# Kernel tuning notes

Hardware: AMD Instinct MI355X
Metric: run time of the kernel (lower is better)

The kernel has to match this reference:

```python
import jax, jax.numpy as jnp
import numpy as np

N, E, F_IN, HID, EMB = 100000, 3200000, 128, 16, 8
NEG_SLOPE = 0.2


def _seg_softmax(logits, seg, n):
    # Numerically stable softmax over segments (per trailing channel if 2D).
    m = jax.ops.segment_max(logits, seg, num_segments=n)
    e = jnp.exp(logits - m[seg])
    s = jax.ops.segment_sum(e, seg, num_segments=n)
    return e / s[seg]


def _gatv2(x, src, dst, Wl, Wr, att, bias, t, n):
    # GATv2Conv, heads=1, add_self_loops=False, eval mode (dropout off),
    # with learnable SoftmaxAggregation replacing the sum aggregation.
    xl = x @ Wl                      # [N, C] source transform
    xr = x @ Wr                      # [N, C] target transform
    score = jnp.sum(jax.nn.leaky_relu(xl[src] + xr[dst], NEG_SLOPE) * att, axis=-1)  # [E]
    alpha = _seg_softmax(score, dst, n)          # attention softmax over incoming edges
    m = xl[src] * alpha[:, None]                 # [E, C] messages
    w = _seg_softmax(m * t, dst, n)              # SoftmaxAggregation(learn=True), per channel
    return jax.ops.segment_sum(w * m, dst, num_segments=n) + bias


def setup_inputs() -> dict:
    key = jax.random.key(0)
    ks = iter(jax.random.split(key, 32))
    r = lambda shape, s=0.1: jax.random.normal(next(ks), shape, dtype=jnp.float32) * s
    return dict(
        x=r((N, F_IN), 1.0),
        edge_index=jax.random.randint(next(ks), (2, E), 0, N, dtype=jnp.int32),
        batch=jnp.arange(N, dtype=jnp.int32),
        Wl1=r((F_IN, HID)), Wr1=r((F_IN, HID)), att1=r((HID,)), b1=r((HID,)),
        Wlin1=r((F_IN, HID)), blin1=r((HID,)),
        Wl2=r((HID, EMB)), Wr2=r((HID, EMB)), att2=r((EMB,)), b2=r((EMB,)),
        Wlin2=r((HID, EMB)), blin2=r((EMB,)),
        t=jnp.ones((1,), jnp.float32),
        W3=r((EMB, EMB)), b3=r((EMB,)),
        W4=r((EMB, 1)), b4=r((1,)),
        W5=r((1, 1)), b5=r((1,)),
        Wout=r((1, 1)), bout=r((1,)),
    )


def reference(x, edge_index, batch, Wl1, Wr1, att1, b1, Wlin1, blin1,
              Wl2, Wr2, att2, b2, Wlin2, blin2, t,
              W3, b3, W4, b4, W5, b5, Wout, bout):
    n = x.shape[0]
    src, dst = edge_index[0], edge_index[1]
    # layer 1: GATv2 + skip Linear, relu, global_add_pool
    h = _gatv2(x, src, dst, Wl1, Wr1, att1, b1, t, n) + (x @ Wlin1 + blin1)
    h = jax.nn.relu(h)
    g = jax.ops.segment_sum(h, batch, num_segments=n)  # global_add_pool (batch=arange(N))
    # layer 2: GATv2 + skip Linear on pooled tensor (as in original code), relu, pool
    h2 = _gatv2(g, src, dst, Wl2, Wr2, att2, b2, t, n) + (g @ Wlin2 + blin2)
    h2 = jax.nn.relu(h2)
    g2 = jax.ops.segment_sum(h2, batch, num_segments=n)
    # small MLP head
    z = jax.nn.relu(g2 @ W3 + b3)
    z = jax.nn.relu(z @ W4 + b4)
    z = jax.nn.relu(z @ W5 + b5)
    return jax.nn.log_sigmoid(z @ Wout + bout)
```

## Files before the change

kernel.cpp:

```cpp
#include <hip/hip_runtime.h>
#include <hip/hip_bf16.h>
#include <math.h>

#define F_IN 128
#define C1 16
#define C2 8

#define LBITS 8
#define LOCAL (1 << LBITS)
#define NB_MAX 512
#define ITEMS 16
#define EPB (256 * ITEMS)
#define HISTBLK 512

static __device__ __forceinline__ unsigned short f2bf(float f) {
  __hip_bfloat16 h = __float2bfloat16(f);
  return *(unsigned short*)&h;
}

__global__ __launch_bounds__(256) void hist_gemm(
    const int* __restrict__ dst, int* __restrict__ bcount, int E, int NB,
    const float* __restrict__ x, const float* __restrict__ Wl, const float* __restrict__ Wr,
    const float* __restrict__ Wlin, const float* __restrict__ blin,
    __hip_bfloat16* __restrict__ XLh, float* __restrict__ XR, float* __restrict__ SK, int N) {
  if (blockIdx.x < HISTBLK) {
    __shared__ int h[NB_MAX];
    for (int i = threadIdx.x; i < NB; i += blockDim.x) h[i] = 0;
    __syncthreads();
    int stride = HISTBLK * 256;
    int tid = blockIdx.x * 256 + threadIdx.x;
    if ((E & 3) == 0) {
      const int4* d4 = (const int4*)dst;
      int n4 = E >> 2;
      for (int i = tid; i < n4; i += stride) {
        int4 d = d4[i];
        atomicAdd(&h[d.x >> LBITS], 1);
        atomicAdd(&h[d.y >> LBITS], 1);
        atomicAdd(&h[d.z >> LBITS], 1);
        atomicAdd(&h[d.w >> LBITS], 1);
      }
    } else {
      for (int e = tid; e < E; e += stride) atomicAdd(&h[dst[e] >> LBITS], 1);
    }
    __syncthreads();
    for (int i = threadIdx.x; i < NB; i += blockDim.x)
      if (h[i]) atomicAdd(&bcount[i], h[i]);
  } else {
    int bx = blockIdx.x - HISTBLK;
    int mat = bx % 3;
    int node = (bx / 3) * 256 + threadIdx.x;
    if (node >= N) return;
    const float* __restrict__ W = (mat == 0) ? Wl : (mat == 1) ? Wr : Wlin;
    const float4* xr4 = (const float4*)(x + (size_t)node * F_IN);
    float acc[16];
#pragma unroll
    for (int c = 0; c < 16; c++) acc[c] = 0.f;
#pragma unroll 8
    for (int kk = 0; kk < F_IN / 4; kk++) {
      float4 xv = xr4[kk];
      float xs[4] = {xv.x, xv.y, xv.z, xv.w};
#pragma unroll
      for (int j = 0; j < 4; j++) {
        int k = kk * 4 + j;
#pragma unroll
        for (int c = 0; c < 16; c++) acc[c] = fmaf(xs[j], W[k * 16 + c], acc[c]);
      }
    }
    if (mat == 0) {
      unsigned int pk[8];
#pragma unroll
      for (int i = 0; i < 8; i++)
        pk[i] = (unsigned)f2bf(acc[2 * i]) | ((unsigned)f2bf(acc[2 * i + 1]) << 16);
      uint4* xlp = (uint4*)(XLh + (size_t)node * 16);
      xlp[0] = make_uint4(pk[0], pk[1], pk[2], pk[3]);
      xlp[1] = make_uint4(pk[4], pk[5], pk[6], pk[7]);
    } else if (mat == 1) {
      float4* xrp = (float4*)(XR + (size_t)node * 16);
#pragma unroll
      for (int q = 0; q < 4; q++)
        xrp[q] = make_float4(acc[4 * q], acc[4 * q + 1], acc[4 * q + 2], acc[4 * q + 3]);
    } else {
      float4* skp = (float4*)(SK + (size_t)node * 16);
#pragma unroll
      for (int q = 0; q < 4; q++)
        skp[q] = make_float4(acc[4 * q] + blin[4 * q], acc[4 * q + 1] + blin[4 * q + 1],
                             acc[4 * q + 2] + blin[4 * q + 2], acc[4 * q + 3] + blin[4 * q + 3]);
    }
  }
}

__global__ void bucket_scan(const int* __restrict__ bcount, int* __restrict__ bbase,
                            int* __restrict__ bcursor, int NB) {
  __shared__ int sd[NB_MAX];
  int t = threadIdx.x;
  int v = (t < NB) ? bcount[t] : 0;
  sd[t] = v;
  __syncthreads();
  int acc = v;
  for (int off = 1; off < NB_MAX; off <<= 1) {
    int u = (t >= off) ? sd[t - off] : 0;
    __syncthreads();
    acc += u;
    sd[t] = acc;
    __syncthreads();
  }
  if (t < NB) {
    int excl = acc - v;
    bbase[t] = excl;
    bcursor[t] = excl;
    if (t == NB - 1) bbase[NB] = acc;
  }
}

__global__ __launch_bounds__(256) void phaseA_lds(const int* __restrict__ src,
                                                  const int* __restrict__ dst,
                                                  int* __restrict__ bcursor,
                                                  int* __restrict__ packed, int E, int NB) {
  __shared__ int hist[NB_MAX];
  __shared__ int lbase[NB_MAX];
  __shared__ int gbase[NB_MAX];
  __shared__ int sdata[256];
  __shared__ int stage[EPB];
  __shared__ unsigned short stageb[EPB];
  int t = threadIdx.x;
  for (int i = t; i < NB; i += 256) hist[i] = 0;
  __syncthreads();
  int base = blockIdx.x * EPB;
  int vals[ITEMS];
  int bkt[ITEMS];
  bool vec = ((E & 3) == 0) && (base + EPB <= E);
  if (vec) {
    const int4* s4 = (const int4*)(src + base);
    const int4* d4 = (const int4*)(dst + base);
#pragma unroll
    for (int q = 0; q < ITEMS / 4; q++) {
      int idx = q * 256 + t;
      int4 sv = s4[idx];
      int4 dv = d4[idx];
      int ss[4] = {sv.x, sv.y, sv.z, sv.w};
      int dd[4] = {dv.x, dv.y, dv.z, dv.w};
#pragma unroll
      for (int r = 0; r < 4; r++) {
        int k = q * 4 + r;
        bkt[k] = dd[r] >> LBITS;
        vals[k] = (ss[r] << LBITS) | (dd[r] & (LOCAL - 1));
        atomicAdd(&hist[bkt[k]], 1);
      }
    }
  } else {
#pragma unroll
    for (int k = 0; k < ITEMS; k++) {
      int e = base + k * 256 + t;
      if (e < E) {
        int s = src[e];
        int d = dst[e];
        bkt[k] = d >> LBITS;
        vals[k] = (s << LBITS) | (d & (LOCAL - 1));
        atomicAdd(&hist[bkt[k]], 1);
      } else {
        bkt[k] = -1;
      }
    }
  }
  __syncthreads();
  int i0 = 2 * t, i1 = 2 * t + 1;
  int h0 = (i0 < NB) ? hist[i0] : 0;
  int h1 = (i1 < NB) ? hist[i1] : 0;
  int s2 = h0 + h1;
  sdata[t] = s2;
  __syncthreads();
  int acc = s2;
  for (int off = 1; off < 256; off <<= 1) {
    int u = (t >= off) ? sdata[t - off] : 0;
    __syncthreads();
    acc += u;
    sdata[t] = acc;
    __syncthreads();
  }
  int excl = acc - s2;
  if (i0 < NB) lbase[i0] = excl;
  if (i1 < NB) lbase[i1] = excl + h0;
  __syncthreads();
  for (int i = t; i < NB; i += 256) {
    int c = hist[i];
    gbase[i] = c ? atomicAdd(&bcursor[i], c) : 0;
    hist[i] = lbase[i];
  }
  __syncthreads();
  if (vec) {
#pragma unroll
    for (int k = 0; k < ITEMS; k++) {
      int lp = atomicAdd(&hist[bkt[k]], 1);
      stage[lp] = vals[k];
      stageb[lp] = (unsigned short)bkt[k];
    }
  } else {
#pragma unroll
    for (int k = 0; k < ITEMS; k++) {
      if (bkt[k] >= 0) {
        int lp = atomicAdd(&hist[bkt[k]], 1);
        stage[lp] = vals[k];
        stageb[lp] = (unsigned short)bkt[k];
      }
    }
  }
  __syncthreads();
  int blockE = E - base;
  if (blockE > EPB) blockE = EPB;
  for (int i = t; i < blockE; i += 256) {
    int b = stageb[i];
    packed[gbase[b] + (i - lbase[b])] = stage[i];
  }
}

__global__ void phaseB_sort(const int* __restrict__ packed, const int* __restrict__ bbase,
                            int* __restrict__ row_ptr, int* __restrict__ ssrc, int N, int E) {
  __shared__ int h[LOCAL];
  __shared__ int sd[LOCAL];
  int b = blockIdx.x;
  int t = threadIdx.x;
  int beg = bbase[b], end = bbase[b + 1];
  int node0 = b << LBITS;
  h[t] = 0;
  __syncthreads();
  for (int j = beg + t; j < end; j += blockDim.x) atomicAdd(&h[packed[j] & (LOCAL - 1)], 1);
  __syncthreads();
  int cnt = h[t];
  sd[t] = cnt;
  __syncthreads();
  int acc = cnt;
  for (int off = 1; off < LOCAL; off <<= 1) {
    int u = (t >= off) ? sd[t - off] : 0;
    __syncthreads();
    acc += u;
    sd[t] = acc;
    __syncthreads();
  }
  int myex = acc - cnt;
  int node = node0 + t;
  if (node < N) row_ptr[node] = beg + myex;
  h[t] = beg + myex;
  if (b == gridDim.x - 1 && t == 0) row_ptr[N] = E;
  __syncthreads();
  for (int j = beg + t; j < end; j += blockDim.x) {
    int v = packed[j];
    int l = v & (LOCAL - 1);
    int p = atomicAdd(&h[l], 1);
    ssrc[p] = ((v >> LBITS) << 5) | (l & 31);
  }
}

template <int C, int POOL, bool HEAD, bool FUSEG2>
__global__ __launch_bounds__(256) void gat_layer(
    const __hip_bfloat16* __restrict__ XLh, const float* __restrict__ XR,
    const float* __restrict__ SK, const float* __restrict__ att, const float* __restrict__ bias,
    const float* __restrict__ tp, const int* __restrict__ row_ptr, const int* __restrict__ ssrc,
    float* __restrict__ H, int N,
    const float* __restrict__ P0, const float* __restrict__ P1, const float* __restrict__ P2,
    const float* __restrict__ P3, const float* __restrict__ P4, const float* __restrict__ P5,
    const float* __restrict__ P6, const float* __restrict__ P7,
    __hip_bfloat16* __restrict__ XL2h, float* __restrict__ XR2, float* __restrict__ SK2,
    float* __restrict__ out) {
  constexpr int NPB = 256 / C;
  __shared__ __align__(16) unsigned short vpool[POOL * C];
  __shared__ float ppool[POOL];
  __shared__ __align__(16) float xrl[NPB * C];
  __shared__ int nb[NPB + 1];
  __shared__ float wfuse[FUSEG2 ? 392 : 1];
  float* hsh = (float*)vpool;
  int t = threadIdx.x;
  int node0 = blockIdx.x * NPB;

  if (t <= NPB) {
    int nd = node0 + t;
    nb[t] = row_ptr[(nd < N) ? nd : N];
  }
  {
    size_t xi = (size_t)node0 * C + t;
    xrl[t] = (xi < (size_t)N * C) ? XR[xi] : 0.f;
  }
  if constexpr (FUSEG2) {
    for (int i = t; i < 392; i += 256)
      wfuse[i] = (i < 128) ? P0[i] : (i < 256) ? P1[i - 128] : (i < 384) ? P2[i - 256] : P3[i - 384];
  }
  float attr[C];
#pragma unroll
  for (int cc = 0; cc < C; cc++) attr[cc] = att[cc];
  float tval = tp[0];
  __syncthreads();

  int bbeg = nb[0];
  int nE = nb[NPB] - bbeg;
  int nCap = (nE < POOL) ? nE : POOL;
  const unsigned short* XLu = (const unsigned short*)XLh;

  for (int slot = t; slot < nCap; slot += 256) {
    int sp = ssrc[bbeg + slot];
    int s = sp >> 5;
    int g = sp & (NPB - 1);
    float v[C];
    if constexpr (C == 16) {
      const uint4* gp = (const uint4*)(XLu + (size_t)s * 16);
      uint4 a = gp[0], b = gp[1];
      *(uint4*)&vpool[slot * 16] = a;
      *(uint4*)&vpool[slot * 16 + 8] = b;
      unsigned arr[8] = {a.x, a.y, a.z, a.w, b.x, b.y, b.z, b.w};
#pragma unroll
      for (int i = 0; i < 8; i++) {
        v[2 * i] = __uint_as_float(arr[i] << 16);
        v[2 * i + 1] = __uint_as_float(arr[i] & 0xffff0000u);
      }
    } else {
      const uint4* gp = (const uint4*)(XLu + (size_t)s * 8);
      uint4 a = gp[0];
      *(uint4*)&vpool[slot * 8] = a;
      unsigned arr[4] = {a.x, a.y, a.z, a.w};
#pragma unroll
      for (int i = 0; i < 4; i++) {
        v[2 * i] = __uint_as_float(arr[i] << 16);
        v[2 * i + 1] = __uint_as_float(arr[i] & 0xffff0000u);
      }
    }
    float xr[C];
    const float4* xp = (const float4*)&xrl[g * C];
#pragma unroll
    for (int q = 0; q < C / 4; q++) {
      float4 f = xp[q];
      xr[4 * q] = f.x;
      xr[4 * q + 1] = f.y;
      xr[4 * q + 2] = f.z;
      xr[4 * q + 3] = f.w;
    }
    float p0 = 0.f, p1 = 0.f, p2 = 0.f, p3 = 0.f;
#pragma unroll
    for (int cc = 0; cc < C; cc += 4) {
      float u0 = v[cc] + xr[cc];
      float u1 = v[cc + 1] + xr[cc + 1];
      float u2 = v[cc + 2] + xr[cc + 2];
      float u3 = v[cc + 3] + xr[cc + 3];
      p0 = fmaf(fmaxf(u0, 0.2f * u0), attr[cc], p0);
      p1 = fmaf(fmaxf(u1, 0.2f * u1), attr[cc + 1], p1);
      p2 = fmaf(fmaxf(u2, 0.2f * u2), attr[cc + 2], p2);
      p3 = fmaf(fmaxf(u3, 0.2f * u3), attr[cc + 3], p3);
    }
    ppool[slot] = __expf((p0 + p1) + (p2 + p3));
  }
  __syncthreads();

  int g = t / C;
  int c = t % C;
  int base = nb[g] - bbeg;
  int deg = nb[g + 1] - nb[g];
  int capd = POOL - base;
  capd = capd < 0 ? 0 : (capd > deg ? deg : capd);

  float invS0;
  {
    float s0 = 0.f;
    for (int j = c; j < capd; j += C) s0 += ppool[base + j];
    for (int j = capd + c; j < deg; j += C) {
      int s = ssrc[bbeg + base + j] >> 5;
      float sc = 0.f;
#pragma unroll
      for (int cc = 0; cc < C; cc++) {
        float v = __bfloat162float(XLh[(size_t)s * C + cc]);
        float u = v + xrl[g * C + cc];
        sc = fmaf(fmaxf(u, 0.2f * u), attr[cc], sc);
      }
      s0 += __expf(sc);
    }
#pragma unroll
    for (int m = 1; m < C; m <<= 1) s0 += __shfl_xor(s0, m, C);
    invS0 = (deg > 0) ? 1.0f / s0 : 0.f;
  }
  float a = invS0 * tval;

  float S1 = 0.f, S2 = 0.f, S1b = 0.f, S2b = 0.f;
  int jj = 0;
  for (; jj + 2 <= capd; jj += 2) {
    int sl0 = base + jj;
    float v0 = __uint_as_float(((unsigned)vpool[sl0 * C + c]) << 16);
    float q0 = v0 * ppool[sl0] * a;
    float v1 = __uint_as_float(((unsigned)vpool[(sl0 + 1) * C + c]) << 16);
    float q1 = v1 * ppool[sl0 + 1] * a;
    float w0 = __expf(q0);
    float w1 = __expf(q1);
    S1 += w0;
    S2 = fmaf(w0, q0, S2);
    S1b += w1;
    S2b = fmaf(w1, q1, S2b);
  }
  for (; jj < capd; jj++) {
    int sl = base + jj;
    float v = __uint_as_float(((unsigned)vpool[sl * C + c]) << 16);
    float q = v * ppool[sl] * a;
    float w = __expf(q);
    S1 += w;
    S2 = fmaf(w, q, S2);
  }
  for (; jj < deg; jj++) {
    int s = ssrc[bbeg + base + jj] >> 5;
    float sc = 0.f, vc = 0.f;
#pragma unroll
    for (int cc = 0; cc < C; cc++) {
      float v = __bfloat162float(XLh[(size_t)s * C + cc]);
      if (cc == c) vc = v;
      float u = v + xrl[g * C + cc];
      sc = fmaf(fmaxf(u, 0.2f * u), attr[cc], sc);
    }
    float p = __expf(sc);
    float q = vc * p * a;
    float w = __expf(q);
    S1 += w;
    S2 = fmaf(w, q, S2);
  }
  S1 += S1b;
  S2 += S2b;

  int node = node0 + g;
  bool valid = node < N;
  float hval = 0.f;
  if (valid) {
    float td = (tval != 0.f) ? tval : 1.f;
    float gat = (deg > 0) ? (S2 / (S1 * td)) : 0.f;
    hval = fmaxf(gat + bias[c] + SK[(size_t)node * C + c], 0.f);
  }
  if constexpr (FUSEG2) {
    __syncthreads();
    hsh[g * C + c] = hval;
    __syncthreads();
    if (t < NPB * 8) {
      int g2 = t >> 3, c2 = t & 7;
      int nd = node0 + g2;
      if (nd < N) {
        float a0 = 0.f, a1 = 0.f, a2 = 0.f;
#pragma unroll
        for (int k = 0; k < 16; k++) {
          float hv = hsh[g2 * 16 + k];
          a0 = fmaf(hv, wfuse[k * 8 + c2], a0);
          a1 = fmaf(hv, wfuse[128 + k * 8 + c2], a1);
          a2 = fmaf(hv, wfuse[256 + k * 8 + c2], a2);
        }
        ((unsigned short*)XL2h)[(size_t)nd * 8 + c2] = f2bf(a0);
        XR2[(size_t)nd * 8 + c2] = a1;
        SK2[(size_t)nd * 8 + c2] = a2 + wfuse[384 + c2];
      }
    }
  } else if constexpr (HEAD) {
    __syncthreads();
    hsh[g * C + c] = hval;
    __syncthreads();
    if (t < NPB) {
      int nd = node0 + t;
      if (nd < N) {
        float h[8];
#pragma unroll
        for (int k = 0; k < 8; k++) h[k] = hsh[t * 8 + k];
        float s4 = 0.f;
#pragma unroll
        for (int cc = 0; cc < 8; cc++) {
          float z = P1[cc];
#pragma unroll
          for (int k = 0; k < 8; k++) z = fmaf(h[k], P0[k * 8 + cc], z);
          z = fmaxf(z, 0.f);
          s4 = fmaf(z, P2[cc], s4);
        }
        s4 = fmaxf(s4 + P3[0], 0.f);
        float s5 = fmaxf(fmaf(s4, P4[0], P5[0]), 0.f);
        float zo = fmaf(s5, P6[0], P7[0]);
        float ls;
        if (zo >= 0.f)
          ls = -log1pf(expf(-zo));
        else
          ls = zo - log1pf(expf(zo));
        out[nd] = ls;
      }
    }
  } else {
    if (valid) H[(size_t)node * C + c] = hval;
  }
}

extern "C" void kernel_launch(void* const* d_in, const int* in_sizes, int n_in,
                              void* d_out, int out_size, void* d_ws, size_t ws_size,
                              hipStream_t stream) {
  const float* x = (const float*)d_in[0];
  const int* ei = (const int*)d_in[1];
  const float* Wl1 = (const float*)d_in[3];
  const float* Wr1 = (const float*)d_in[4];
  const float* att1 = (const float*)d_in[5];
  const float* b1 = (const float*)d_in[6];
  const float* Wlin1 = (const float*)d_in[7];
  const float* blin1 = (const float*)d_in[8];
  const float* Wl2 = (const float*)d_in[9];
  const float* Wr2 = (const float*)d_in[10];
  const float* att2 = (const float*)d_in[11];
  const float* b2 = (const float*)d_in[12];
  const float* Wlin2 = (const float*)d_in[13];
  const float* blin2 = (const float*)d_in[14];
  const float* t = (const float*)d_in[15];
  const float* W3 = (const float*)d_in[16];
  const float* b3 = (const float*)d_in[17];
  const float* W4 = (const float*)d_in[18];
  const float* b4 = (const float*)d_in[19];
  const float* W5 = (const float*)d_in[20];
  const float* b5 = (const float*)d_in[21];
  const float* Wout = (const float*)d_in[22];
  const float* bout = (const float*)d_in[23];
  float* out = (float*)d_out;

  int N = in_sizes[0] / F_IN;
  int E = in_sizes[1] / 2;
  const int* src = ei;
  const int* dst = ei + E;
  int NB = (N + LOCAL - 1) >> LBITS;

  char* ws = (char*)d_ws;
  size_t off = 0;
  auto alloc = [&](size_t bytes) -> void* {
    void* p = ws + off;
    off = (off + bytes + 255) & ~(size_t)255;
    return p;
  };
  int* bcount = (int*)alloc((size_t)NB * 4);
  int* bbase = (int*)alloc((size_t)(NB + 1) * 4);
  int* bcursor = (int*)alloc((size_t)NB * 4);
  int* packed = (int*)alloc((size_t)E * 4);
  int* row_ptr = (int*)alloc((size_t)(N + 1) * 4);
  int* ssrc = (int*)alloc((size_t)E * 4);
  __hip_bfloat16* XL1 = (__hip_bfloat16*)alloc((size_t)N * C1 * 2);
  float* XR1 = (float*)alloc((size_t)N * C1 * 4);
  float* SK1 = (float*)alloc((size_t)N * C1 * 4);
  __hip_bfloat16* XL2 = (__hip_bfloat16*)alloc((size_t)N * C2 * 2);
  float* XR2 = (float*)alloc((size_t)N * C2 * 4);
  float* SK2 = (float*)alloc((size_t)N * C2 * 4);

  int nblkA = (E + EPB - 1) / EPB;
  int nodeBlk = (N + 255) / 256;

  hipMemsetAsync(bcount, 0, (size_t)NB * 4, stream);
  hipLaunchKernelGGL(hist_gemm, dim3(HISTBLK + nodeBlk * 3), dim3(256), 0, stream, dst, bcount, E,
                     NB, x, Wl1, Wr1, Wlin1, blin1, XL1, XR1, SK1, N);
  hipLaunchKernelGGL(bucket_scan, dim3(1), dim3(NB_MAX), 0, stream, bcount, bbase, bcursor, NB);
  hipLaunchKernelGGL(phaseA_lds, dim3(nblkA), dim3(256), 0, stream, src, dst, bcursor, packed, E,
                     NB);
  hipLaunchKernelGGL(phaseB_sort, dim3(NB), dim3(LOCAL), 0, stream, packed, bbase, row_ptr, ssrc, N,
                     E);
  hipLaunchKernelGGL((gat_layer<16, 576, false, true>), dim3((N + 15) / 16), dim3(256), 0, stream,
                     XL1, XR1, SK1, att1, b1, t, row_ptr, ssrc, nullptr, N, Wl2, Wr2, Wlin2, blin2,
                     nullptr, nullptr, nullptr, nullptr, XL2, XR2, SK2, nullptr);
  hipLaunchKernelGGL((gat_layer<8, 1216, true, false>), dim3((N + 31) / 32), dim3(256), 0, stream,
                     XL2, XR2, SK2, att2, b2, t, row_ptr, ssrc, nullptr, N, W3, b3, W4, b4, W5, b5,
                     Wout, bout, nullptr, nullptr, nullptr, out);
}
```

Measured before the change: 302.7 us.

## Stage x rows in LDS and compute all three projections per block

The node GEMM in hist_gemm now loads a 64-node tile of x once into transposed, padded shared memory. Three wavefronts (192 threads) each compute one of Wl, Wr or Wlin for those rows, so x is no longer read from global memory three times by separate blocks, and the weight index is made wave-uniform via readfirstlane. The gat_layer kernel gets a dedicated hsh buffer instead of aliasing vpool, which removes one barrier, and the layer-1 POOL size is raised. The 33KB static LDS array now also applies to the histogram blocks, which may reduce their occupancy.

```diff
diff --git a/kernel.cpp b/kernel.cpp
--- a/kernel.cpp
+++ b/kernel.cpp
@@ -18,17 +18,19 @@
   return *(unsigned short*)&h;
 }
 
-__global__ __launch_bounds__(256) void hist_gemm(
+__global__ __launch_bounds__(192) void hist_gemm(
     const int* __restrict__ dst, int* __restrict__ bcount, int E, int NB,
     const float* __restrict__ x, const float* __restrict__ Wl, const float* __restrict__ Wr,
     const float* __restrict__ Wlin, const float* __restrict__ blin,
     __hip_bfloat16* __restrict__ XLh, float* __restrict__ XR, float* __restrict__ SK, int N) {
+  __shared__ float smem[128 * 65];
+  int t = threadIdx.x;
   if (blockIdx.x < HISTBLK) {
-    __shared__ int h[NB_MAX];
-    for (int i = threadIdx.x; i < NB; i += blockDim.x) h[i] = 0;
-    __syncthreads();
-    int stride = HISTBLK * 256;
-    int tid = blockIdx.x * 256 + threadIdx.x;
+    int* h = (int*)smem;
+    for (int i = t; i < NB; i += blockDim.x) h[i] = 0;
+    __syncthreads();
+    int stride = HISTBLK * blockDim.x;
+    int tid = blockIdx.x * blockDim.x + t;
     if ((E & 3) == 0) {
       const int4* d4 = (const int4*)dst;
       int n4 = E >> 2;
@@ -43,48 +45,59 @@
       for (int e = tid; e < E; e += stride) atomicAdd(&h[dst[e] >> LBITS], 1);
     }
     __syncthreads();
-    for (int i = threadIdx.x; i < NB; i += blockDim.x)
+    for (int i = t; i < NB; i += blockDim.x)
       if (h[i]) atomicAdd(&bcount[i], h[i]);
   } else {
     int bx = blockIdx.x - HISTBLK;
-    int mat = bx % 3;
-    int node = (bx / 3) * 256 + threadIdx.x;
-    if (node >= N) return;
-    const float* __restrict__ W = (mat == 0) ? Wl : (mat == 1) ? Wr : Wlin;
-    const float4* xr4 = (const float4*)(x + (size_t)node * F_IN);
+    int node0 = bx * 64;
+    int nrem = N - node0;
+    if (nrem > 64) nrem = 64;
+    int row = t & 63;
+    int cg = t >> 6;
+    if (row < nrem) {
+      const float4* xr4 = (const float4*)(x + (size_t)(node0 + row) * F_IN);
+      for (int cc = cg; cc < 32; cc += 3) {
+        float4 v = xr4[cc];
+        smem[(cc * 4 + 0) * 65 + row] = v.x;
+        smem[(cc * 4 + 1) * 65 + row] = v.y;
+        smem[(cc * 4 + 2) * 65 + row] = v.z;
+        smem[(cc * 4 + 3) * 65 + row] = v.w;
+      }
+    }
+    __syncthreads();
+    int cgu = __builtin_amdgcn_readfirstlane(cg);
+    const float* __restrict__ W = (cgu == 0) ? Wl : (cgu == 1) ? Wr : Wlin;
     float acc[16];
 #pragma unroll
     for (int c = 0; c < 16; c++) acc[c] = 0.f;
-#pragma unroll 8
-    for (int kk = 0; kk < F_IN / 4; kk++) {
-      float4 xv = xr4[kk];
-      float xs[4] = {xv.x, xv.y, xv.z, xv.w};
-#pragma unroll
-      for (int j = 0; j < 4; j++) {
-        int k = kk * 4 + j;
-#pragma unroll
-        for (int c = 0; c < 16; c++) acc[c] = fmaf(xs[j], W[k * 16 + c], acc[c]);
-      }
-    }
-    if (mat == 0) {
-      unsigned int pk[8];
-#pragma unroll
-      for (int i = 0; i < 8; i++)
-        pk[i] = (unsigned)f2bf(acc[2 * i]) | ((unsigned)f2bf(acc[2 * i + 1]) << 16);
-      uint4* xlp = (uint4*)(XLh + (size_t)node * 16);
-      xlp[0] = make_uint4(pk[0], pk[1], pk[2], pk[3]);
-      xlp[1] = make_uint4(pk[4], pk[5], pk[6], pk[7]);
-    } else if (mat == 1) {
-      float4* xrp = (float4*)(XR + (size_t)node * 16);
-#pragma unroll
-      for (int q = 0; q < 4; q++)
-        xrp[q] = make_float4(acc[4 * q], acc[4 * q + 1], acc[4 * q + 2], acc[4 * q + 3]);
-    } else {
-      float4* skp = (float4*)(SK + (size_t)node * 16);
-#pragma unroll
-      for (int q = 0; q < 4; q++)
-        skp[q] = make_float4(acc[4 * q] + blin[4 * q], acc[4 * q + 1] + blin[4 * q + 1],
-                             acc[4 * q + 2] + blin[4 * q + 2], acc[4 * q + 3] + blin[4 * q + 3]);
+#pragma unroll 4
+    for (int k = 0; k < F_IN; k++) {
+      float xv = smem[k * 65 + row];
+#pragma unroll
+      for (int c = 0; c < 16; c++) acc[c] = fmaf(xv, W[k * 16 + c], acc[c]);
+    }
+    if (row < nrem) {
+      int node = node0 + row;
+      if (cgu == 0) {
+        unsigned int pk[8];
+#pragma unroll
+        for (int i = 0; i < 8; i++)
+          pk[i] = (unsigned)f2bf(acc[2 * i]) | ((unsigned)f2bf(acc[2 * i + 1]) << 16);
+        uint4* xlp = (uint4*)(XLh + (size_t)node * 16);
+        xlp[0] = make_uint4(pk[0], pk[1], pk[2], pk[3]);
+        xlp[1] = make_uint4(pk[4], pk[5], pk[6], pk[7]);
+      } else if (cgu == 1) {
+        float4* xrp = (float4*)(XR + (size_t)node * 16);
+#pragma unroll
+        for (int q = 0; q < 4; q++)
+          xrp[q] = make_float4(acc[4 * q], acc[4 * q + 1], acc[4 * q + 2], acc[4 * q + 3]);
+      } else {
+        float4* skp = (float4*)(SK + (size_t)node * 16);
+#pragma unroll
+        for (int q = 0; q < 4; q++)
+          skp[q] = make_float4(acc[4 * q] + blin[4 * q], acc[4 * q + 1] + blin[4 * q + 1],
+                               acc[4 * q + 2] + blin[4 * q + 2], acc[4 * q + 3] + blin[4 * q + 3]);
+      }
     }
   }
 }
@@ -266,8 +279,8 @@
   __shared__ float ppool[POOL];
   __shared__ __align__(16) float xrl[NPB * C];
   __shared__ int nb[NPB + 1];
+  __shared__ float hsh[(HEAD || FUSEG2) ? NPB * C : 1];
   __shared__ float wfuse[FUSEG2 ? 392 : 1];
-  float* hsh = (float*)vpool;
   int t = threadIdx.x;
   int node0 = blockIdx.x * NPB;
 
@@ -426,7 +439,6 @@
     hval = fmaxf(gat + bias[c] + SK[(size_t)node * C + c], 0.f);
   }
   if constexpr (FUSEG2) {
-    __syncthreads();
     hsh[g * C + c] = hval;
     __syncthreads();
     if (t < NPB * 8) {
@@ -447,7 +459,6 @@
       }
     }
   } else if constexpr (HEAD) {
-    __syncthreads();
     hsh[g * C + c] = hval;
     __syncthreads();
     if (t < NPB) {
@@ -536,17 +547,17 @@
   float* SK2 = (float*)alloc((size_t)N * C2 * 4);
 
   int nblkA = (E + EPB - 1) / EPB;
-  int nodeBlk = (N + 255) / 256;
+  int nodeBlk64 = (N + 63) / 64;
 
   hipMemsetAsync(bcount, 0, (size_t)NB * 4, stream);
-  hipLaunchKernelGGL(hist_gemm, dim3(HISTBLK + nodeBlk * 3), dim3(256), 0, stream, dst, bcount, E,
+  hipLaunchKernelGGL(hist_gemm, dim3(HISTBLK + nodeBlk64), dim3(192), 0, stream, dst, bcount, E,
                      NB, x, Wl1, Wr1, Wlin1, blin1, XL1, XR1, SK1, N);
   hipLaunchKernelGGL(bucket_scan, dim3(1), dim3(NB_MAX), 0, stream, bcount, bbase, bcursor, NB);
   hipLaunchKernelGGL(phaseA_lds, dim3(nblkA), dim3(256), 0, stream, src, dst, bcursor, packed, E,
                      NB);
   hipLaunchKernelGGL(phaseB_sort, dim3(NB), dim3(LOCAL), 0, stream, packed, bbase, row_ptr, ssrc, N,
                      E);
-  hipLaunchKernelGGL((gat_layer<16, 576, false, true>), dim3((N + 15) / 16), dim3(256), 0, stream,
+  hipLaunchKernelGGL((gat_layer<16, 640, false, true>), dim3((N + 15) / 16), dim3(256), 0, stream,
                      XL1, XR1, SK1, att1, b1, t, row_ptr, ssrc, nullptr, N, Wl2, Wr2, Wlin2, blin2,
                      nullptr, nullptr, nullptr, nullptr, XL2, XR2, SK2, nullptr);
   hipLaunchKernelGGL((gat_layer<8, 1216, true, false>), dim3((N + 31) / 32), dim3(256), 0, stream,
```

After: 307.5 us. No clear change (+1.6%).
